# Kernel optimization log

Hardware: AMD Instinct MI355X
Metric: run time of the kernel (lower is better)

Reference implementation:

```python
import jax, jax.numpy as jnp
import numpy as np

B, S, E, H = 2, 2048, 1024, 16
DH = E // H


def setup_inputs() -> dict:
    key = jax.random.key(0)
    ks = jax.random.split(key, 9)
    s = 1.0 / np.sqrt(E)
    return {
        "queries": jax.random.normal(ks[0], (B, S, E), dtype=jnp.float32),
        "keys": jax.random.normal(ks[1], (B, S, E), dtype=jnp.float32),
        "values": jax.random.normal(ks[2], (B, S, E), dtype=jnp.float32),
        "mask": jax.random.randint(ks[3], (B, 1, 1, S), 0, 2, dtype=jnp.int32),
        "Wq": jax.random.normal(ks[4], (E, E), dtype=jnp.float32) * s,
        "Wk": jax.random.normal(ks[5], (E, E), dtype=jnp.float32) * s,
        "Wv": jax.random.normal(ks[6], (E, E), dtype=jnp.float32) * s,
        "Wo": jax.random.normal(ks[7], (E, E), dtype=jnp.float32) * s,
        "bo": jax.random.normal(ks[8], (E,), dtype=jnp.float32) * s,
    }


def reference(queries, keys, values, mask, Wq, Wk, Wv, Wo, bo):
    n, d_q, _ = queries.shape
    d_k = keys.shape[1]
    # Linear projections (torch Linear: x @ W.T), then split into heads
    q = (queries @ Wq.T).reshape(n, d_q, H, DH)
    k = (keys @ Wk.T).reshape(n, d_k, H, DH)
    v = (values @ Wv.T).reshape(n, d_k, H, DH)
    # [n, H, d_q, d_k] attention scores
    energy = jnp.einsum("nqhd,nkhd->nhqk", q, k)
    energy = jnp.where(mask == 0, jnp.float32(-1e20), energy)
    # NOTE: original scales by sqrt(key seq length), not head dim -- kept faithful
    attn = jax.nn.softmax(energy / jnp.sqrt(jnp.float32(d_k)), axis=3)
    out = jnp.einsum("nhql,nlhd->nqhd", attn, v).reshape(n, d_q, E)
    return out @ Wo.T + bo
```

## Files before the change

kernel.cpp:

```cpp
#include <hip/hip_runtime.h>
#include <hip/hip_bf16.h>

#define BB 2
#define SS 2048
#define EE 1024
#define HH 16
#define DHH 64

using bf16x8 = __attribute__((ext_vector_type(8))) __bf16;
using f32x4  = __attribute__((ext_vector_type(4))) float;
using f32x16 = __attribute__((ext_vector_type(16))) float;
using uint2v = __attribute__((ext_vector_type(2))) unsigned int;

#if __has_builtin(__builtin_amdgcn_exp2f)
#define EXP2(x) __builtin_amdgcn_exp2f(x)
#else
#define EXP2(x) __exp2f(x)
#endif

static __device__ __forceinline__ unsigned short f2bf(float f) {
    unsigned int u = __float_as_uint(f);
    u += 0x7FFFu + ((u >> 16) & 1u);
    return (unsigned short)(u >> 16);
}

static __device__ __forceinline__ unsigned int pk2bf(float lo, float hi) {
    union { __hip_bfloat162 h2; unsigned int u; } c;
    c.h2 = __float22bfloat162_rn(float2{lo, hi});
    return c.u;
}

static __device__ __forceinline__ void async_load16(const void* g, void* l) {
    __builtin_amdgcn_global_load_lds(
        (const __attribute__((address_space(1))) unsigned int*)g,
        (__attribute__((address_space(3))) unsigned int*)l, 16, 0, 0);
}

__global__ void cvt_kernel(const float* __restrict__ W0, const float* __restrict__ W1,
                           const float* __restrict__ W2, const float* __restrict__ W3,
                           const float* __restrict__ X0, const float* __restrict__ X1,
                           const float* __restrict__ X2,
                           unsigned short* __restrict__ Wb,
                           unsigned short* __restrict__ D0, unsigned short* __restrict__ D1,
                           unsigned short* __restrict__ D2)
{
    const int z = blockIdx.y;
    const float* src;
    unsigned short* dst;
    if (z < 4) {
        if (blockIdx.x >= 512) return;
        src = (z == 0) ? W0 : (z == 1) ? W1 : (z == 2) ? W2 : W3;
        dst = Wb + (size_t)z * 1048576;
    } else {
        src = (z == 4) ? X0 : (z == 5) ? X1 : X2;
        dst = (z == 4) ? D0 : (z == 5) ? D1 : D2;
    }
    const size_t base = (size_t)blockIdx.x * 2048 + (size_t)threadIdx.x * 8;
    const float4 f0 = *(const float4*)(src + base);
    const float4 f1 = *(const float4*)(src + base + 4);
    uint4 p;
    p.x = pk2bf(f0.x, f0.y); p.y = pk2bf(f0.z, f0.w);
    p.z = pk2bf(f1.x, f1.y); p.w = pk2bf(f1.z, f1.w);
    *(uint4*)(dst + base) = p;
}

template<int MT, int NT, bool BF16OUT>
__global__ __launch_bounds__(256, 3)
void gemm_xwt(const unsigned short* __restrict__ X0, const unsigned short* __restrict__ X1,
              const unsigned short* __restrict__ X2,
              const unsigned short* __restrict__ W0, const unsigned short* __restrict__ W1,
              const unsigned short* __restrict__ W2,
              void* __restrict__ Y0, void* __restrict__ Y1, void* __restrict__ Y2,
              const float* __restrict__ bias, int M, int N, int K,
              float s0, float s1, float s2)
{
    constexpr int BK = 32;
    constexpr int NI = MT / 32;
    constexpr int NJ = NT / 32;
    __shared__ __align__(16) unsigned short As[2][MT * BK];
    __shared__ __align__(16) unsigned short Bs[2][NT * BK];

    const int z = blockIdx.z;
    const unsigned short* __restrict__ X = (z == 0) ? X0 : ((z == 1) ? X1 : X2);
    const unsigned short* __restrict__ W = (z == 0) ? W0 : ((z == 1) ? W1 : W2);
    void* __restrict__ Y                 = (z == 0) ? Y0 : ((z == 1) ? Y1 : Y2);
    const float ysc                      = (z == 0) ? s0 : ((z == 1) ? s1 : s2);

    const int tid  = threadIdx.x;
    const int lane = tid & 63;
    const int wave = tid >> 6;
    const int wm   = (wave >> 1) * (MT / 2);
    const int wn   = (wave & 1) * (NT / 2);

    const unsigned gx  = gridDim.x;
    const unsigned gy  = gridDim.y;
    const unsigned lin = blockIdx.x + gx * blockIdx.y;
    const unsigned k8  = lin & 7u;
    const unsigned j   = lin >> 3;
    const int m0 = (int)(k8 * (gy >> 3) + j / gx) * MT;
    const int n0 = (int)(j % gx) * NT;

    const int l16  = lane & 15;
    const int quad = lane >> 4;

    const int arow = lane >> 2;
    const int akc  = (lane & 3) * 8;

    f32x4 acc[NI][NJ];
    #pragma unroll
    for (int i = 0; i < NI; i++)
        #pragma unroll
        for (int j2 = 0; j2 < NJ; j2++) acc[i][j2] = f32x4{0.f, 0.f, 0.f, 0.f};

    auto stage = [&](int k0, int buf) {
        #pragma unroll
        for (int j2 = 0; j2 < NT / 64; j2++) {
            const int rr = wave * (NT / 4) + j2 * 16;
            async_load16(W + (size_t)(n0 + rr + arow) * K + k0 + akc, Bs[buf] + rr * BK);
        }
        #pragma unroll
        for (int j2 = 0; j2 < MT / 64; j2++) {
            const int rr = wave * (MT / 4) + j2 * 16;
            async_load16(X + (size_t)(m0 + rr + arow) * K + k0 + akc, As[buf] + rr * BK);
        }
    };

    stage(0, 0);
    const int niter = K / BK;
    for (int i = 0; i < niter; i++) {
        const int cur = i & 1;
        __syncthreads();
        if (i + 1 < niter) stage((i + 1) * BK, cur ^ 1);

        bf16x8 afrag[NI], bfrag[NJ];
        #pragma unroll
        for (int ii = 0; ii < NI; ii++)
            afrag[ii] = *(const bf16x8*)(As[cur] + (wm + ii * 16 + l16) * BK + quad * 8);
        #pragma unroll
        for (int j2 = 0; j2 < NJ; j2++)
            bfrag[j2] = *(const bf16x8*)(Bs[cur] + (wn + j2 * 16 + l16) * BK + quad * 8);
        #pragma unroll
        for (int ii = 0; ii < NI; ii++)
            #pragma unroll
            for (int j2 = 0; j2 < NJ; j2++)
                acc[ii][j2] = __builtin_amdgcn_mfma_f32_16x16x32_bf16(afrag[ii], bfrag[j2], acc[ii][j2], 0, 0, 0);
    }

    #pragma unroll
    for (int i = 0; i < NI; i++) {
        #pragma unroll
        for (int j2 = 0; j2 < NJ; j2++) {
            #pragma unroll
            for (int r = 0; r < 4; r++) {
                const int row = m0 + wm + i * 16 + quad * 4 + r;
                const int col = n0 + wn + j2 * 16 + l16;
                const float v = acc[i][j2][r];
                if (BF16OUT) {
                    ((unsigned short*)Y)[(size_t)row * N + col] = f2bf(v * ysc);
                } else {
                    ((float*)Y)[(size_t)row * N + col] = v + bias[col];
                }
            }
        }
    }
}

__global__ __launch_bounds__(256, 1)
void compact_kernel(const unsigned short* __restrict__ Kb,
                    const unsigned short* __restrict__ Vb,
                    const int* __restrict__ mask,
                    unsigned short* __restrict__ Kc,
                    unsigned short* __restrict__ Vtc)
{
    constexpr int LDE = 264;
    __shared__ int srcIdx[64];
    __shared__ int wsum[4];
    __shared__ __align__(16) unsigned short T[64 * LDE];

    const int tid  = threadIdx.x;
    const int lane = tid & 63;
    const int wave = tid >> 6;
    const int b    = blockIdx.y;
    const int t0   = blockIdx.x * 64;

    const int base = tid * 8;
    int v[8]; int run = 0;
    #pragma unroll
    for (int i = 0; i < 8; i++) { v[i] = (mask[b * SS + base + i] != 0) ? 1 : 0; run += v[i]; }

    int inc = run;
    #pragma unroll
    for (int d = 1; d < 64; d <<= 1) {
        int n = __shfl_up(inc, d, 64);
        if (lane >= d) inc += n;
    }
    if (lane == 63) wsum[wave] = inc;
    __syncthreads();
    const int nkeep = wsum[0] + wsum[1] + wsum[2] + wsum[3];
    if (t0 >= nkeep) return;

    if (tid < 64) srcIdx[tid] = -1;
    __syncthreads();

    int r = inc - run;
    #pragma unroll
    for (int w = 0; w < 4; w++) if (w < wave) r += wsum[w];
    #pragma unroll
    for (int i = 0; i < 8; i++) {
        if (v[i]) {
            if (r >= t0 && r < t0 + 64) srcIdx[r - t0] = base + i;
            r++;
        }
    }
    __syncthreads();

    {
        const int j = tid >> 2, part = tid & 3;
        const int s = srcIdx[j];
        uint4* dst = (uint4*)(Kc + ((size_t)(b * SS + t0 + j)) * EE + part * 256);
        if (s >= 0) {
            const uint4* src = (const uint4*)(Kb + ((size_t)(b * SS + s)) * EE + part * 256);
            #pragma unroll
            for (int c = 0; c < 32; c++) dst[c] = src[c];
        } else {
            #pragma unroll
            for (int c = 0; c < 32; c++) dst[c] = uint4{0, 0, 0, 0};
        }
    }

    for (int ec = 0; ec < 4; ec++) {
        __syncthreads();
        {
            const int j = tid >> 2, part = tid & 3;
            const int s = srcIdx[j];
            uint4* trow = (uint4*)(T + j * LDE + part * 64);
            if (s >= 0) {
                const uint4* src = (const uint4*)(Vb + ((size_t)(b * SS + s)) * EE + ec * 256 + part * 64);
                #pragma unroll
                for (int c = 0; c < 8; c++) trow[c] = src[c];
            } else {
                #pragma unroll
                for (int c = 0; c < 8; c++) trow[c] = uint4{0, 0, 0, 0};
            }
        }
        __syncthreads();
        {
            const int e = ec * 256 + tid;
            unsigned short* drow = Vtc + ((size_t)(b * EE + e)) * SS + t0;
            unsigned short tmp[64];
            #pragma unroll
            for (int j2 = 0; j2 < 64; j2++) tmp[j2] = T[j2 * LDE + tid];
            #pragma unroll
            for (int c = 0; c < 8; c++) ((uint4*)drow)[c] = ((const uint4*)tmp)[c];
        }
    }
}

__global__ __launch_bounds__(256, 2)
void attn_kernel(const unsigned short* __restrict__ Qb,
                 const unsigned short* __restrict__ Kc,
                 const unsigned short* __restrict__ Vtc,
                 const int* __restrict__ mask,
                 unsigned short* __restrict__ AO)
{
    constexpr int LDK = 68;
    constexpr int LDV = 68;
    __shared__ __align__(16) unsigned short Ks[64 * LDK];
    __shared__ __align__(16) unsigned short Vs[64 * LDV];
    __shared__ float Lsum[4][32];
    __shared__ int nk_s;

    const int tid  = threadIdx.x;
    const int lane = tid & 63;
    const int wave = tid >> 6;
    const int l32  = lane & 31;
    const int hi   = lane >> 5;

    const int linear = blockIdx.x;
    const int bh     = (linear & 7) * 4 + ((linear >> 3) & 3);
    const int qblk   = linear >> 5;
    const int b  = bh >> 4;
    const int h  = bh & 15;
    const int q0 = qblk * 128 + wave * 32;

    if (tid == 0) nk_s = 0;
    __syncthreads();
    {
        int cnt = 0;
        #pragma unroll
        for (int i = 0; i < 8; i++) cnt += (mask[b * SS + tid * 8 + i] != 0) ? 1 : 0;
        #pragma unroll
        for (int d = 32; d >= 1; d >>= 1) cnt += __shfl_xor(cnt, d, 64);
        if (lane == 0) atomicAdd(&nk_s, cnt);
    }
    __syncthreads();
    const int nkeep  = nk_s;
    const int ntiles = (nkeep + 63) >> 6;

    bf16x8 qf[4];
    {
        const unsigned short* qptr = Qb + (size_t)(b * SS + q0 + l32) * EE + h * DHH + hi * 8;
        #pragma unroll
        for (int t = 0; t < 4; t++) qf[t] = *(const bf16x8*)(qptr + t * 16);
    }

    float lsum = 0.f;
    f32x16 o_acc[2];
    #pragma unroll
    for (int d = 0; d < 2; d++)
        #pragma unroll
        for (int r = 0; r < 16; r++) o_acc[d][r] = 0.f;

    const int srow = tid >> 2;
    const int sc   = (tid & 3) * 16;

    uint4 kr0, kr1, vr0, vr1;
    auto gload = [&](int t0) {
        const unsigned short* kg = Kc + (size_t)(b * SS + t0 + srow) * EE + h * DHH + sc;
        kr0 = *(const uint4*)(kg);
        kr1 = *(const uint4*)(kg + 8);
        const unsigned short* vg = Vtc + (size_t)(b * EE + h * DHH + srow) * SS + t0 + sc;
        vr0 = *(const uint4*)(vg);
        vr1 = *(const uint4*)(vg + 8);
    };
    gload(0);

    for (int it = 0; it < ntiles; it++) {
        const int t0 = it * 64;
        __syncthreads();
        *(uint4*)(Ks + srow * LDK + sc)     = kr0;
        *(uint4*)(Ks + srow * LDK + sc + 8) = kr1;
        *(uint4*)(Vs + srow * LDV + sc)     = vr0;
        *(uint4*)(Vs + srow * LDV + sc + 8) = vr1;
        __syncthreads();

        if (it + 1 < ntiles) gload(t0 + 64);

        const bool full = (t0 + 64 <= nkeep);

        #pragma unroll
        for (int blk = 0; blk < 2; blk++) {
            f32x16 s;
            __builtin_amdgcn_s_setprio(1);
            {
                bf16x8 kf = *(const bf16x8*)(Ks + (blk * 32 + l32) * LDK + hi * 8);
                f32x16 z;
                #pragma unroll
                for (int r = 0; r < 16; r++) z[r] = 0.f;
                s = __builtin_amdgcn_mfma_f32_32x32x16_bf16(kf, qf[0], z, 0, 0, 0);
            }
            #pragma unroll
            for (int t = 1; t < 4; t++) {
                bf16x8 kf = *(const bf16x8*)(Ks + (blk * 32 + l32) * LDK + t * 16 + hi * 8);
                s = __builtin_amdgcn_mfma_f32_32x32x16_bf16(kf, qf[t], s, 0, 0, 0);
            }
            __builtin_amdgcn_s_setprio(0);

            float p[16];
            #pragma unroll
            for (int r = 0; r < 16; r++) p[r] = EXP2(s[r]);
            if (!full) {
                const int keyb = t0 + blk * 32 + 4 * hi;
                #pragma unroll
                for (int r = 0; r < 16; r++)
                    if (keyb + ((r & 3) + 8 * (r >> 2)) >= nkeep) p[r] = 0.f;
            }
            #pragma unroll
            for (int r = 0; r < 16; r += 4)
                lsum += ((p[r] + p[r + 1]) + (p[r + 2] + p[r + 3]));

            const unsigned int u0 = pk2bf(p[0],  p[1]);
            const unsigned int u1 = pk2bf(p[2],  p[3]);
            const unsigned int u2 = pk2bf(p[4],  p[5]);
            const unsigned int u3 = pk2bf(p[6],  p[7]);
            const unsigned int u4 = pk2bf(p[8],  p[9]);
            const unsigned int u5 = pk2bf(p[10], p[11]);
            const unsigned int u6 = pk2bf(p[12], p[13]);
            const unsigned int u7 = pk2bf(p[14], p[15]);
            const uint2v s02 = __builtin_amdgcn_permlane32_swap(u0, u2, false, false);
            const uint2v s13 = __builtin_amdgcn_permlane32_swap(u1, u3, false, false);
            const uint2v s46 = __builtin_amdgcn_permlane32_swap(u4, u6, false, false);
            const uint2v s57 = __builtin_amdgcn_permlane32_swap(u5, u7, false, false);

            union { unsigned int u[4]; bf16x8 v; } pa0, pa1;
            pa0.u[0] = s02.x; pa0.u[1] = s13.x; pa0.u[2] = s02.y; pa0.u[3] = s13.y;
            pa1.u[0] = s46.x; pa1.u[1] = s57.x; pa1.u[2] = s46.y; pa1.u[3] = s57.y;

            __builtin_amdgcn_s_setprio(1);
            #pragma unroll
            for (int kc = 0; kc < 2; kc++) {
                const bf16x8 pav = (kc == 0) ? pa0.v : pa1.v;
                #pragma unroll
                for (int dblk = 0; dblk < 2; dblk++) {
                    bf16x8 vf = *(const bf16x8*)(Vs + (dblk * 32 + l32) * LDV + blk * 32 + kc * 16 + hi * 8);
                    o_acc[dblk] = __builtin_amdgcn_mfma_f32_32x32x16_bf16(pav, vf, o_acc[dblk], 0, 0, 0);
                }
            }
            __builtin_amdgcn_s_setprio(0);
        }
    }

    {
        float ls = lsum;
        ls += __shfl_xor(ls, 32, 64);
        Lsum[wave][l32] = 1.0f / ls;
    }
    __builtin_amdgcn_s_waitcnt(0xC07F);

    #pragma unroll
    for (int r = 0; r < 16; r++) {
        const int qr = (r & 3) + 8 * (r >> 2) + 4 * hi;
        const float rl = Lsum[wave][qr];
        const size_t orow = (size_t)(b * SS + q0 + qr) * EE + h * DHH + l32;
        AO[orow]      = f2bf(o_acc[0][r] * rl);
        AO[orow + 32] = f2bf(o_acc[1][r] * rl);
    }
}

extern "C" void kernel_launch(void* const* d_in, const int* in_sizes, int n_in,
                              void* d_out, int out_size, void* d_ws, size_t ws_size,
                              hipStream_t stream)
{
    (void)in_sizes; (void)n_in; (void)out_size; (void)ws_size;
    const float* queries = (const float*)d_in[0];
    const float* keys    = (const float*)d_in[1];
    const float* values  = (const float*)d_in[2];
    const int*   mask    = (const int*)d_in[3];
    const float* Wq      = (const float*)d_in[4];
    const float* Wk      = (const float*)d_in[5];
    const float* Wv      = (const float*)d_in[6];
    const float* Wo      = (const float*)d_in[7];
    const float* bo      = (const float*)d_in[8];

    const size_t NE = (size_t)BB * SS * EE;
    const size_t WE = (size_t)EE * EE;

    unsigned short* Xq  = (unsigned short*)d_out;
    unsigned short* Xk  = Xq + NE;
    unsigned short* Kc  = (unsigned short*)d_out;
    unsigned short* Vtc = Kc + NE;
    unsigned short* Wb  = (unsigned short*)d_ws;
    unsigned short* Xv  = Wb + 4 * WE;
    unsigned short* Qb  = Xv + NE;
    unsigned short* Kb  = Qb + NE;
    unsigned short* Vb  = Kb + NE;
    unsigned short* AOb = Xv;

    const int M = BB * SS, N = EE, K = EE;
    const float qscale = 0.022097086912079608f * 1.4426950408889634f;

    cvt_kernel<<<dim3(2048, 7), 256, 0, stream>>>(
        Wq, Wk, Wv, Wo, queries, keys, values, Wb, Xq, Xk, Xv);

    dim3 gproj(N / 128, M / 128, 3);
    gemm_xwt<128, 128, true><<<gproj, 256, 0, stream>>>(
        Xq, Xk, Xv, Wb, Wb + WE, Wb + 2 * WE,
        (void*)Qb, (void*)Kb, (void*)Vb, nullptr, M, N, K,
        qscale, 1.0f, 1.0f);

    compact_kernel<<<dim3(SS / 64, BB), 256, 0, stream>>>(Kb, Vb, mask, Kc, Vtc);

    attn_kernel<<<dim3(512), 256, 0, stream>>>(Qb, Kc, Vtc, mask, AOb);

    dim3 gout(N / 64, M / 128, 1);
    gemm_xwt<128, 64, false><<<gout, 256, 0, stream>>>(
        AOb, AOb, AOb, Wb + 3 * WE, Wb + 3 * WE, Wb + 3 * WE,
        d_out, d_out, d_out, bo, M, N, K, 1.0f, 1.0f, 1.0f);
}
```

Measured before the change: 219.6 us.

## Compact masked keys before K/V projection and skip projection of masked rows

Masked-out key/value rows are now gathered and compacted from the fp32 inputs before the projection GEMM, fused with bf16 conversion, instead of projecting every row and compacting afterwards. The projection GEMM reads the per-batch kept count from a device global and exits early for K/V tiles beyond it, and the V projection writes its output directly in transposed layout. This removes the separate compact kernel, the transposed copy through shared memory, and roughly half of the K/V projection FLOPs when about half the mask is zero. In exchange it relies on a global device variable written by one block, and adds uint2 transposed stores that may be poorly coalesced.

```diff
diff --git a/kernel.cpp b/kernel.cpp
--- a/kernel.cpp
+++ b/kernel.cpp
@@ -18,6 +18,8 @@
 #define EXP2(x) __exp2f(x)
 #endif
 
+__device__ int g_nkeep[2];
+
 static __device__ __forceinline__ unsigned short f2bf(float f) {
     unsigned int u = __float_as_uint(f);
     u += 0x7FFFu + ((u >> 16) & 1u);
@@ -38,11 +40,9 @@
 
 __global__ void cvt_kernel(const float* __restrict__ W0, const float* __restrict__ W1,
                            const float* __restrict__ W2, const float* __restrict__ W3,
-                           const float* __restrict__ X0, const float* __restrict__ X1,
-                           const float* __restrict__ X2,
+                           const float* __restrict__ Xqs,
                            unsigned short* __restrict__ Wb,
-                           unsigned short* __restrict__ D0, unsigned short* __restrict__ D1,
-                           unsigned short* __restrict__ D2)
+                           unsigned short* __restrict__ Dq)
 {
     const int z = blockIdx.y;
     const float* src;
@@ -52,8 +52,8 @@
         src = (z == 0) ? W0 : (z == 1) ? W1 : (z == 2) ? W2 : W3;
         dst = Wb + (size_t)z * 1048576;
     } else {
-        src = (z == 4) ? X0 : (z == 5) ? X1 : X2;
-        dst = (z == 4) ? D0 : (z == 5) ? D1 : D2;
+        src = Xqs;
+        dst = Dq;
     }
     const size_t base = (size_t)blockIdx.x * 2048 + (size_t)threadIdx.x * 8;
     const float4 f0 = *(const float4*)(src + base);
@@ -62,6 +62,76 @@
     p.x = pk2bf(f0.x, f0.y); p.y = pk2bf(f0.z, f0.w);
     p.z = pk2bf(f1.x, f1.y); p.w = pk2bf(f1.z, f1.w);
     *(uint4*)(dst + base) = p;
+}
+
+__global__ __launch_bounds__(256, 2)
+void gather_kernel(const float* __restrict__ Ksrc, const float* __restrict__ Vsrc,
+                   const int* __restrict__ mask,
+                   unsigned short* __restrict__ Xkc, unsigned short* __restrict__ Xvc)
+{
+    __shared__ int srcIdx[64];
+    __shared__ int wsum[4];
+
+    const int tid  = threadIdx.x;
+    const int lane = tid & 63;
+    const int wave = tid >> 6;
+    const int b    = blockIdx.y;
+    const int t0   = blockIdx.x * 64;
+    const float* __restrict__ src = blockIdx.z ? Vsrc : Ksrc;
+    unsigned short* __restrict__ dst = blockIdx.z ? Xvc : Xkc;
+
+    const int base = tid * 8;
+    int v[8]; int run = 0;
+    #pragma unroll
+    for (int i = 0; i < 8; i++) { v[i] = (mask[b * SS + base + i] != 0) ? 1 : 0; run += v[i]; }
+
+    int inc = run;
+    #pragma unroll
+    for (int d = 1; d < 64; d <<= 1) {
+        int n = __shfl_up(inc, d, 64);
+        if (lane >= d) inc += n;
+    }
+    if (lane == 63) wsum[wave] = inc;
+    __syncthreads();
+    const int nkeep = wsum[0] + wsum[1] + wsum[2] + wsum[3];
+
+    if (blockIdx.x == 0 && blockIdx.z == 0 && tid == 0) g_nkeep[b] = nkeep;
+
+    if (t0 >= ((nkeep + 127) & ~127)) return;
+
+    if (tid < 64) srcIdx[tid] = -1;
+    __syncthreads();
+
+    int r = inc - run;
+    #pragma unroll
+    for (int w = 0; w < 4; w++) if (w < wave) r += wsum[w];
+    #pragma unroll
+    for (int i = 0; i < 8; i++) {
+        if (v[i]) {
+            if (r >= t0 && r < t0 + 64) srcIdx[r - t0] = base + i;
+            r++;
+        }
+    }
+    __syncthreads();
+
+    const int j = tid >> 2, part = tid & 3;
+    const int s = srcIdx[j];
+    unsigned short* drow = dst + ((size_t)(b * SS + t0 + j)) * EE + part * 256;
+    if (s >= 0) {
+        const float* srow = src + ((size_t)(b * SS + s)) * EE + part * 256;
+        #pragma unroll
+        for (int c = 0; c < 32; c++) {
+            const float4 f0 = *(const float4*)(srow + c * 8);
+            const float4 f1 = *(const float4*)(srow + c * 8 + 4);
+            uint4 p;
+            p.x = pk2bf(f0.x, f0.y); p.y = pk2bf(f0.z, f0.w);
+            p.z = pk2bf(f1.x, f1.y); p.w = pk2bf(f1.z, f1.w);
+            *(uint4*)(drow + c * 8) = p;
+        }
+    } else {
+        #pragma unroll
+        for (int c = 0; c < 32; c++) *(uint4*)(drow + c * 8) = uint4{0, 0, 0, 0};
+    }
 }
 
 template<int MT, int NT, bool BF16OUT>
@@ -100,6 +170,11 @@
     const int m0 = (int)(k8 * (gy >> 3) + j / gx) * MT;
     const int n0 = (int)(j % gx) * NT;
 
+    if (BF16OUT && z > 0) {
+        const int bb = m0 >> 11;
+        if ((m0 & 2047) >= g_nkeep[bb]) return;
+    }
+
     const int l16  = lane & 15;
     const int quad = lane >> 4;
 
@@ -146,112 +221,38 @@
                 acc[ii][j2] = __builtin_amdgcn_mfma_f32_16x16x32_bf16(afrag[ii], bfrag[j2], acc[ii][j2], 0, 0, 0);
     }
 
-    #pragma unroll
-    for (int i = 0; i < NI; i++) {
-        #pragma unroll
-        for (int j2 = 0; j2 < NJ; j2++) {
-            #pragma unroll
-            for (int r = 0; r < 4; r++) {
-                const int row = m0 + wm + i * 16 + quad * 4 + r;
-                const int col = n0 + wn + j2 * 16 + l16;
-                const float v = acc[i][j2][r];
-                if (BF16OUT) {
-                    ((unsigned short*)Y)[(size_t)row * N + col] = f2bf(v * ysc);
-                } else {
-                    ((float*)Y)[(size_t)row * N + col] = v + bias[col];
+    if (BF16OUT && z == 2) {
+        #pragma unroll
+        for (int i = 0; i < NI; i++) {
+            #pragma unroll
+            for (int j2 = 0; j2 < NJ; j2++) {
+                const int row  = m0 + wm + i * 16 + quad * 4;
+                const int bb   = row >> 11;
+                const int slot = row & 2047;
+                const int col  = n0 + wn + j2 * 16 + l16;
+                uint2 pck;
+                pck.x = pk2bf(acc[i][j2][0], acc[i][j2][1]);
+                pck.y = pk2bf(acc[i][j2][2], acc[i][j2][3]);
+                *(uint2*)((unsigned short*)Y + ((size_t)(bb * EE + col)) * SS + slot) = pck;
+            }
+        }
+    } else {
+        #pragma unroll
+        for (int i = 0; i < NI; i++) {
+            #pragma unroll
+            for (int j2 = 0; j2 < NJ; j2++) {
+                #pragma unroll
+                for (int r = 0; r < 4; r++) {
+                    const int row = m0 + wm + i * 16 + quad * 4 + r;
+                    const int col = n0 + wn + j2 * 16 + l16;
+                    const float v = acc[i][j2][r];
+                    if (BF16OUT) {
+                        ((unsigned short*)Y)[(size_t)row * N + col] = f2bf(v * ysc);
+                    } else {
+                        ((float*)Y)[(size_t)row * N + col] = v + bias[col];
+                    }
                 }
             }
-        }
-    }
-}
-
-__global__ __launch_bounds__(256, 1)
-void compact_kernel(const unsigned short* __restrict__ Kb,
-                    const unsigned short* __restrict__ Vb,
-                    const int* __restrict__ mask,
-                    unsigned short* __restrict__ Kc,
-                    unsigned short* __restrict__ Vtc)
-{
-    constexpr int LDE = 264;
-    __shared__ int srcIdx[64];
-    __shared__ int wsum[4];
-    __shared__ __align__(16) unsigned short T[64 * LDE];
-
-    const int tid  = threadIdx.x;
-    const int lane = tid & 63;
-    const int wave = tid >> 6;
-    const int b    = blockIdx.y;
-    const int t0   = blockIdx.x * 64;
-
-    const int base = tid * 8;
-    int v[8]; int run = 0;
-    #pragma unroll
-    for (int i = 0; i < 8; i++) { v[i] = (mask[b * SS + base + i] != 0) ? 1 : 0; run += v[i]; }
-
-    int inc = run;
-    #pragma unroll
-    for (int d = 1; d < 64; d <<= 1) {
-        int n = __shfl_up(inc, d, 64);
-        if (lane >= d) inc += n;
-    }
-    if (lane == 63) wsum[wave] = inc;
-    __syncthreads();
-    const int nkeep = wsum[0] + wsum[1] + wsum[2] + wsum[3];
-    if (t0 >= nkeep) return;
-
-    if (tid < 64) srcIdx[tid] = -1;
-    __syncthreads();
-
-    int r = inc - run;
-    #pragma unroll
-    for (int w = 0; w < 4; w++) if (w < wave) r += wsum[w];
-    #pragma unroll
-    for (int i = 0; i < 8; i++) {
-        if (v[i]) {
-            if (r >= t0 && r < t0 + 64) srcIdx[r - t0] = base + i;
-            r++;
-        }
-    }
-    __syncthreads();
-
-    {
-        const int j = tid >> 2, part = tid & 3;
-        const int s = srcIdx[j];
-        uint4* dst = (uint4*)(Kc + ((size_t)(b * SS + t0 + j)) * EE + part * 256);
-        if (s >= 0) {
-            const uint4* src = (const uint4*)(Kb + ((size_t)(b * SS + s)) * EE + part * 256);
-            #pragma unroll
-            for (int c = 0; c < 32; c++) dst[c] = src[c];
-        } else {
-            #pragma unroll
-            for (int c = 0; c < 32; c++) dst[c] = uint4{0, 0, 0, 0};
-        }
-    }
-
-    for (int ec = 0; ec < 4; ec++) {
-        __syncthreads();
-        {
-            const int j = tid >> 2, part = tid & 3;
-            const int s = srcIdx[j];
-            uint4* trow = (uint4*)(T + j * LDE + part * 64);
-            if (s >= 0) {
-                const uint4* src = (const uint4*)(Vb + ((size_t)(b * SS + s)) * EE + ec * 256 + part * 64);
-                #pragma unroll
-                for (int c = 0; c < 8; c++) trow[c] = src[c];
-            } else {
-                #pragma unroll
-                for (int c = 0; c < 8; c++) trow[c] = uint4{0, 0, 0, 0};
-            }
-        }
-        __syncthreads();
-        {
-            const int e = ec * 256 + tid;
-            unsigned short* drow = Vtc + ((size_t)(b * EE + e)) * SS + t0;
-            unsigned short tmp[64];
-            #pragma unroll
-            for (int j2 = 0; j2 < 64; j2++) tmp[j2] = T[j2 * LDE + tid];
-            #pragma unroll
-            for (int c = 0; c < 8; c++) ((uint4*)drow)[c] = ((const uint4*)tmp)[c];
         }
     }
 }
@@ -435,30 +436,30 @@
     const size_t NE = (size_t)BB * SS * EE;
     const size_t WE = (size_t)EE * EE;
 
+    unsigned short* Wb  = (unsigned short*)d_ws;
+    unsigned short* Qb  = Wb + 4 * WE;
+    unsigned short* Kc  = Qb + NE;
+    unsigned short* Vtc = Kc + NE;
+    unsigned short* Xvc = Vtc + NE;
+    unsigned short* AOb = Xvc;
+
     unsigned short* Xq  = (unsigned short*)d_out;
-    unsigned short* Xk  = Xq + NE;
-    unsigned short* Kc  = (unsigned short*)d_out;
-    unsigned short* Vtc = Kc + NE;
-    unsigned short* Wb  = (unsigned short*)d_ws;
-    unsigned short* Xv  = Wb + 4 * WE;
-    unsigned short* Qb  = Xv + NE;
-    unsigned short* Kb  = Qb + NE;
-    unsigned short* Vb  = Kb + NE;
-    unsigned short* AOb = Xv;
+    unsigned short* Xkc = Xq + NE;
 
     const int M = BB * SS, N = EE, K = EE;
     const float qscale = 0.022097086912079608f * 1.4426950408889634f;
 
-    cvt_kernel<<<dim3(2048, 7), 256, 0, stream>>>(
-        Wq, Wk, Wv, Wo, queries, keys, values, Wb, Xq, Xk, Xv);
+    cvt_kernel<<<dim3(2048, 5), 256, 0, stream>>>(
+        Wq, Wk, Wv, Wo, queries, Wb, Xq);
+
+    gather_kernel<<<dim3(SS / 64, BB, 2), 256, 0, stream>>>(
+        keys, values, mask, Xkc, Xvc);
 
     dim3 gproj(N / 128, M / 128, 3);
     gemm_xwt<128, 128, true><<<gproj, 256, 0, stream>>>(
-        Xq, Xk, Xv, Wb, Wb + WE, Wb + 2 * WE,
-        (void*)Qb, (void*)Kb, (void*)Vb, nullptr, M, N, K,
+        Xq, Xkc, Xvc, Wb, Wb + WE, Wb + 2 * WE,
+        (void*)Qb, (void*)Kc, (void*)Vtc, nullptr, M, N, K,
         qscale, 1.0f, 1.0f);
-
-    compact_kernel<<<dim3(SS / 64, BB), 256, 0, stream>>>(Kb, Vb, mask, Kc, Vtc);
 
     attn_kernel<<<dim3(512), 256, 0, stream>>>(Qb, Kc, Vtc, mask, AOb);
 
```

Measured after the change: 217.8 us. No clear change (-0.8%).
